# Kernel tuning notes

Hardware: AMD Instinct MI355X
Metric: run time of the kernel (lower is better)

Reference implementation:

```python
import jax, jax.numpy as jnp
import numpy as np

# Constants from init_kwargs
DT = 0.01
NIV = 8          # energy_input_dim[1]
HID = 64         # hidden_dims[0]
FEAT = 501       # per-field microstructure feature length (501+501=1002)


def _lin(k, fin, fout):
    return jax.random.normal(k, (fin, fout), dtype=jnp.float32) / np.sqrt(fin)


def setup_inputs() -> dict:
    key = jax.random.key(0)
    ks = jax.random.split(key, 12)
    B, T = 8192, 512
    e = jax.random.normal(ks[0], (B, T, 1), dtype=jnp.float32) * 0.1
    e_dot = jax.random.normal(ks[1], (B, T, 1), dtype=jnp.float32) * 0.1
    # positive microstructure fields (code computes nu**-1 and E/nu**2)
    E = jax.random.uniform(ks[2], (B, FEAT), minval=0.5, maxval=2.0, dtype=jnp.float32)
    nu = jax.random.uniform(ks[3], (B, FEAT), minval=0.5, maxval=2.0, dtype=jnp.float32)
    return {
        "e": e, "e_dot": e_dot, "E": E, "nu": nu,
        # EnergyFunction.B : Linear(1002,64) -> ReLU -> Linear(64,niv)
        "Bw1": _lin(ks[4], 2 * FEAT, HID), "Bb1": jnp.zeros((HID,), jnp.float32),
        "Bw2": _lin(ks[5], HID, NIV), "Bb2": jnp.zeros((NIV,), jnp.float32),
        # InverseDissipationPotential.beta : Linear(1002,64)->Softplus->Linear(64,niv)->Softplus
        "bw1": _lin(ks[6], 2 * FEAT, HID), "bb1": jnp.zeros((HID,), jnp.float32),
        "bw2": _lin(ks[7], HID, NIV), "bb2": jnp.zeros((NIV,), jnp.float32),
    }


def reference(e, e_dot, E, nu, Bw1, Bb1, Bw2, Bb2, bw1, bb1, bw2, bb2):
    # --- microstructure encoder (TrueFeatures) ---
    nu_p = 1.0 / jnp.mean(1.0 / nu, axis=1, keepdims=True)                 # [B,1]
    E_p = jnp.mean(E / nu ** 2, axis=1, keepdims=True) * nu_p ** 2         # [B,1]
    m = jnp.concatenate([E, nu], axis=-1)                                  # [B,1002]

    # Time-invariant MLP coefficients (hoisted out of the time loop)
    Bm = jax.nn.relu(m @ Bw1 + Bb1) @ Bw2 + Bb2                            # [B,NIV]
    beta = jax.nn.softplus(jax.nn.softplus(m @ bw1 + bb1) @ bw2 + bb2)     # [B,NIV]
    Bsum = jnp.sum(Bm, axis=-1, keepdims=True)                             # [B,1]

    B_, niv = Bm.shape
    xi0 = jnp.zeros((B_, niv), dtype=e.dtype)

    def step(xi, inp):
        u, p = inp                                                          # [B,1],[B,1]
        # Analytic gradients of L = sum_{b,k} Bm_bk * (0.5*E' u^2 + 0.5*(u-xi_k)^2 + 0.5*sum_j xi_j^2)
        du = u - xi                                                         # [B,NIV]
        grad_u = Bsum * E_p * u + jnp.sum(Bm * du, axis=-1, keepdims=True)  # [B,1] (s_eq)
        grad_v = -Bm * du + Bsum * xi                                       # [B,NIV] (d)
        q = -grad_v
        # Analytic gradients of potential = -0.5*nu' p^2 + 0.5*sum(beta*q^2)
        grad_p = -nu_p * p                                                  # [B,1] (s_neq)
        grad_q = beta * q                                                   # [B,NIV] (kinetics)
        stress = grad_u - grad_p
        return xi + DT * grad_q, (stress, xi)

    xs = (jnp.swapaxes(e, 0, 1), jnp.swapaxes(e_dot, 0, 1))                 # [T,B,1]
    _, (stress_t, xi_t) = jax.lax.scan(step, xi0, xs)
    stress = jnp.swapaxes(stress_t, 0, 1)                                   # [B,T,1]
    xi = jnp.swapaxes(xi_t, 0, 1)                                           # [B,T,NIV]
    return stress, xi
```

## Files before the change

kernel.cpp:

```cpp
#include <hip/hip_runtime.h>
#include <hip/hip_bf16.h>

#define FEATN 501
#define KPAD 1024
#define MSTRIDE 1032
#define NB 8192
#define NT 512
#define DTC 0.01f

typedef __attribute__((ext_vector_type(8))) short short8;
typedef __attribute__((ext_vector_type(4))) float f32x4;

__device__ __forceinline__ float softplus_f(float x) {
    return fmaxf(x, 0.f) + log1pf(expf(-fabsf(x)));
}
__device__ __forceinline__ ushort f2bf(float x) {
    __hip_bfloat16 h = __float2bfloat16(x);
    return *reinterpret_cast<ushort*>(&h);
}
__device__ __forceinline__ void gl_lds16(const void* g, void* l) {
    __builtin_amdgcn_global_load_lds(
        (const __attribute__((address_space(1))) void*)g,
        (__attribute__((address_space(3))) void*)l, 16, 0, 0);
}
__device__ __forceinline__ float dpp_add(float x, const int ctrl) {
    int s = __builtin_bit_cast(int, x);
    int y;
    switch (ctrl) {
    case 0xB1:  y = __builtin_amdgcn_update_dpp(0, s, 0xB1, 0xf, 0xf, true); break;
    case 0x4E:  y = __builtin_amdgcn_update_dpp(0, s, 0x4E, 0xf, 0xf, true); break;
    default:    y = __builtin_amdgcn_update_dpp(0, s, 0x141, 0xf, 0xf, true); break;
    }
    return x + __builtin_bit_cast(float, y);
}

__global__ __launch_bounds__(256) void wtrans_kernel(
    const float* __restrict__ Bw1, const float* __restrict__ bw1,
    ushort* __restrict__ Wt) {
    const int h = blockIdx.x;
    const float* W = (h < 64) ? Bw1 : bw1;
    const int col = h & 63;
    #pragma unroll
    for (int it = 0; it < 4; ++it) {
        const int k = it * 256 + threadIdx.x;
        const int ksrc = (k < FEATN) ? k
                       : (k >= 512 && k < 512 + FEATN) ? k - 11 : -1;
        const float v = (ksrc >= 0) ? W[(size_t)ksrc * 64 + col] : 0.f;
        Wt[(size_t)(((k >> 5) * 128 + h) * 4 + ((k >> 3) & 3)) * 8 + (k & 7)] =
            f2bf(v);
    }
}

__global__ __launch_bounds__(256, 8) void enc_kernel(
    const float* __restrict__ E, const float* __restrict__ nu,
    const ushort* __restrict__ Wt,
    const float* __restrict__ Bb1, const float* __restrict__ bb1,
    const float* __restrict__ Bw2, const float* __restrict__ Bb2,
    const float* __restrict__ bw2, const float* __restrict__ bb2,
    float* __restrict__ cw) {
    __shared__ ushort Ml[8 * MSTRIDE];
    __shared__ float hid[128][9];
    __shared__ float nups[8], Eps[8];

    const int tid = threadIdx.x;
    const int w = tid >> 6, lane = tid & 63;
    const int bb0 = blockIdx.x * 8;

    #pragma unroll
    for (int bp = 0; bp < 2; ++bp) {
        const int bl = w * 2 + bp;
        const size_t base = (size_t)(bb0 + bl) * FEATN;
        float s1 = 0.f, s2 = 0.f;
        for (int i = lane; i < FEATN; i += 64) {
            const float Ev = E[base + i];
            const float nv = nu[base + i];
            const float inv = 1.0f / nv;
            s1 += inv;
            s2 = fmaf(Ev, inv * inv, s2);
            Ml[bl * MSTRIDE + i] = f2bf(Ev);
            Ml[bl * MSTRIDE + 512 + i] = f2bf(nv);
        }
        if (lane < 11) {
            Ml[bl * MSTRIDE + FEATN + lane] = 0;
            Ml[bl * MSTRIDE + 512 + FEATN + lane] = 0;
        }
        #pragma unroll
        for (int o = 32; o; o >>= 1) {
            s1 += __shfl_xor(s1, o);
            s2 += __shfl_xor(s2, o);
        }
        if (lane == 0) {
            const float np = (float)FEATN / s1;
            nups[bl] = np;
            Eps[bl] = (s2 / (float)FEATN) * np * np;
        }
    }
    __syncthreads();

    const int r15 = lane & 15, kg = lane >> 4;
    {
        const ushort* wp = Wt + (size_t)(w * 32 + r15) * 32 + kg * 8;
        const int boff = (r15 & 7) * MSTRIDE + kg * 8;

        f32x4 acc0 = {0.f, 0.f, 0.f, 0.f}, acc1 = acc0;
        #pragma unroll 4
        for (int s = 0; s < 32; ++s) {
            const short8 a0 = *(const short8*)(wp + (size_t)s * 4096);
            const short8 a1 = *(const short8*)(wp + (size_t)s * 4096 + 512);
            const short8 b = *(const short8*)&Ml[boff + s * 32];
            acc0 = __builtin_amdgcn_mfma_f32_16x16x32_bf16(a0, b, acc0, 0, 0, 0);
            acc1 = __builtin_amdgcn_mfma_f32_16x16x32_bf16(a1, b, acc1, 0, 0, 0);
        }
        if (r15 < 8) {
            #pragma unroll
            for (int t = 0; t < 2; ++t) {
                #pragma unroll
                for (int r = 0; r < 4; ++r) {
                    const int h = w * 32 + t * 16 + kg * 4 + r;
                    const float bias = (h < 64) ? Bb1[h] : bb1[h - 64];
                    float v = (t ? acc1[r] : acc0[r]) + bias;
                    v = (h < 64) ? fmaxf(v, 0.f) : softplus_f(v);
                    hid[h][r15] = v;
                }
            }
        }
    }
    __syncthreads();

    if (tid < 64) {
        const int bl = tid >> 3, k = tid & 7;
        float dB = 0.f, db = 0.f;
        #pragma unroll 8
        for (int h = 0; h < 64; ++h) {
            dB = fmaf(hid[h][bl], Bw2[h * 8 + k], dB);
            db = fmaf(hid[64 + h][bl], bw2[h * 8 + k], db);
        }
        const float Bm = dB + Bb2[k];
        const float be = softplus_f(db + bb2[k]);
        float Bs = Bm;
        Bs += __shfl_xor(Bs, 1);
        Bs += __shfl_xor(Bs, 2);
        Bs += __shfl_xor(Bs, 4);
        float* cb = cw + (size_t)(bb0 + bl) * 32;
        cb[k] = 1.f - DTC * be * (Bm + Bs);
        cb[8 + k] = DTC * be * Bm;
        cb[16 + k] = Bm;
        if (k == 0) {
            cb[24] = Bs * (Eps[bl] + 1.f);
            cb[25] = nups[bl];
        }
    }
}

__global__ __launch_bounds__(256) void time_kernel(
    const float* __restrict__ e, const float* __restrict__ ed,
    const float* __restrict__ cw, float* __restrict__ stress,
    float* __restrict__ xi_out) {
    __shared__ float els[4][512];
    __shared__ float pls[4][512];
    const int wv = threadIdx.x >> 6;
    const int wid = (blockIdx.x << 2) + wv;
    const int lane = threadIdx.x & 63;
    const int j = lane >> 3, k = lane & 7;

    const float* eb = e + (size_t)wid * NT;
    const float* edb = ed + (size_t)wid * NT;
    gl_lds16(eb + lane * 4, &els[wv][0]);
    gl_lds16(eb + 256 + lane * 4, &els[wv][256]);
    gl_lds16(edb + lane * 4, &pls[wv][0]);
    gl_lds16(edb + 256 + lane * 4, &pls[wv][256]);

    const float* cb = cw + (size_t)wid * 32;
    const float a = cb[k];
    const float c = cb[8 + k];
    const float Bm = cb[16 + k];
    const float sE2 = cb[24];
    const float nup = cb[25];
    asm volatile("s_waitcnt vmcnt(0)" ::: "memory");

    const float a2 = a * a, a4 = a2 * a2;
    float A = 1.f;
    if (j & 1) A *= a;
    if (j & 2) A *= a2;
    if (j & 4) A *= a4;
    float pw[8];
    {
        float run = c;
        #pragma unroll
        for (int i = 7; i >= 0; --i) {
            const bool on = (i < j);
            pw[i] = on ? run : 0.f;
            run = on ? run * a : run;
        }
    }

    float* xb = xi_out + (size_t)wid * (NT * 8);
    float* sb = stress + (size_t)wid * NT;
    const float* el = &els[wv][0];
    const float* pl = &pls[wv][0];

    float xs = 0.f;
    #pragma unroll
    for (int it = 0; it < 64; ++it) {
        const int t0 = it * 8;
        const float4 q0 = *(const float4*)(el + t0);
        const float4 q1 = *(const float4*)(el + t0 + 4);
        const float cuj = el[t0 + j];
        const float cpj = pl[t0 + j];
        float xi_j = A * xs;
        xi_j = fmaf(pw[0], q0.x, xi_j);
        xi_j = fmaf(pw[1], q0.y, xi_j);
        xi_j = fmaf(pw[2], q0.z, xi_j);
        xi_j = fmaf(pw[3], q0.w, xi_j);
        xi_j = fmaf(pw[4], q1.x, xi_j);
        xi_j = fmaf(pw[5], q1.y, xi_j);
        xi_j = fmaf(pw[6], q1.z, xi_j);
        xi_j = fmaf(pw[7], q1.w, xi_j);
        xb[t0 * 8 + lane] = xi_j;
        float r = Bm * xi_j;
        r = dpp_add(r, 0xB1);
        r = dpp_add(r, 0x4E);
        r = dpp_add(r, 0x141);
        if (k == 0)
            sb[t0 + j] = fmaf(cuj, sE2, fmaf(nup, cpj, -r));
        xs = fmaf(a, __shfl(xi_j, 56 + k), c * q1.w);
    }
}

extern "C" void kernel_launch(void* const* d_in, const int* in_sizes, int n_in,
                              void* d_out, int out_size, void* d_ws, size_t ws_size,
                              hipStream_t stream) {
    const float* e   = (const float*)d_in[0];
    const float* ed  = (const float*)d_in[1];
    const float* E   = (const float*)d_in[2];
    const float* nu  = (const float*)d_in[3];
    const float* Bw1 = (const float*)d_in[4];
    const float* Bb1 = (const float*)d_in[5];
    const float* Bw2 = (const float*)d_in[6];
    const float* Bb2 = (const float*)d_in[7];
    const float* bw1 = (const float*)d_in[8];
    const float* bb1 = (const float*)d_in[9];
    const float* bw2 = (const float*)d_in[10];
    const float* bb2 = (const float*)d_in[11];

    float* out = (float*)d_out;
    float* stress = out;
    float* xi = out + (size_t)NB * NT;
    ushort* Wt = (ushort*)d_ws;
    float* cw = (float*)((char*)d_ws + (1 << 20));

    wtrans_kernel<<<128, 256, 0, stream>>>(Bw1, bw1, Wt);
    enc_kernel<<<1024, 256, 0, stream>>>(E, nu, Wt, Bb1, bb1,
                                         Bw2, Bb2, bw2, bb2, cw);
    time_kernel<<<2048, 256, 0, stream>>>(e, ed, cw, stress, xi);
}
```

Before: 69.29 us.

## Fuse encoder MLP and time-scan kernels into one per-block kernel

Merges the microstructure encoder and the time recurrence into a single kernel where each block handles four batch rows, passing coefficients through shared memory instead of a global workspace. Shared memory is aliased between the encoder staging buffers and the e/e_dot time-series buffers. The MFMA loop now wastes more of each 16-wide tile (only 4 of 16 columns used), and it rotates the K-slice start per block to spread weight reads. This removes a kernel launch and a global round trip, but doubles the per-row weight traffic and lowers the occupancy target.

```diff
diff --git a/kernel.cpp b/kernel.cpp
--- a/kernel.cpp
+++ b/kernel.cpp
@@ -2,8 +2,7 @@
 #include <hip/hip_bf16.h>
 
 #define FEATN 501
-#define KPAD 1024
-#define MSTRIDE 1032
+#define MST4 1032
 #define NB 8192
 #define NT 512
 #define DTC 0.01f
@@ -51,25 +50,29 @@
     }
 }
 
-__global__ __launch_bounds__(256, 8) void enc_kernel(
+__global__ __launch_bounds__(256, 6) void fused_kernel(
     const float* __restrict__ E, const float* __restrict__ nu,
     const ushort* __restrict__ Wt,
     const float* __restrict__ Bb1, const float* __restrict__ bb1,
     const float* __restrict__ Bw2, const float* __restrict__ Bb2,
     const float* __restrict__ bw2, const float* __restrict__ bb2,
-    float* __restrict__ cw) {
-    __shared__ ushort Ml[8 * MSTRIDE];
-    __shared__ float hid[128][9];
-    __shared__ float nups[8], Eps[8];
+    const float* __restrict__ e, const float* __restrict__ ed,
+    float* __restrict__ stress, float* __restrict__ xi_out) {
+    __shared__ __align__(16) char LDSU[16640];
+    ushort* Ml = (ushort*)LDSU;
+    float* hid = (float*)(LDSU + 8320);
+    float* els = (float*)LDSU;
+    float* pls = (float*)(LDSU + 8192);
+    __shared__ float coefL[4][32];
+    __shared__ float nups[4], Eps[4];
 
     const int tid = threadIdx.x;
     const int w = tid >> 6, lane = tid & 63;
-    const int bb0 = blockIdx.x * 8;
-
-    #pragma unroll
-    for (int bp = 0; bp < 2; ++bp) {
-        const int bl = w * 2 + bp;
-        const size_t base = (size_t)(bb0 + bl) * FEATN;
+    const int bb0 = blockIdx.x * 4;
+    const int r15 = lane & 15, kg = lane >> 4;
+
+    {
+        const size_t base = (size_t)(bb0 + w) * FEATN;
         float s1 = 0.f, s2 = 0.f;
         for (int i = lane; i < FEATN; i += 64) {
             const float Ev = E[base + i];
@@ -77,12 +80,12 @@
             const float inv = 1.0f / nv;
             s1 += inv;
             s2 = fmaf(Ev, inv * inv, s2);
-            Ml[bl * MSTRIDE + i] = f2bf(Ev);
-            Ml[bl * MSTRIDE + 512 + i] = f2bf(nv);
+            Ml[w * MST4 + i] = f2bf(Ev);
+            Ml[w * MST4 + 512 + i] = f2bf(nv);
         }
         if (lane < 11) {
-            Ml[bl * MSTRIDE + FEATN + lane] = 0;
-            Ml[bl * MSTRIDE + 512 + FEATN + lane] = 0;
+            Ml[w * MST4 + FEATN + lane] = 0;
+            Ml[w * MST4 + 512 + FEATN + lane] = 0;
         }
         #pragma unroll
         for (int o = 32; o; o >>= 1) {
@@ -91,27 +94,28 @@
         }
         if (lane == 0) {
             const float np = (float)FEATN / s1;
-            nups[bl] = np;
-            Eps[bl] = (s2 / (float)FEATN) * np * np;
+            nups[w] = np;
+            Eps[w] = (s2 / (float)FEATN) * np * np;
         }
     }
     __syncthreads();
 
-    const int r15 = lane & 15, kg = lane >> 4;
     {
-        const ushort* wp = Wt + (size_t)(w * 32 + r15) * 32 + kg * 8;
-        const int boff = (r15 & 7) * MSTRIDE + kg * 8;
+        const int aoff = (w * 32 + r15) * 32 + kg * 8;
+        const int boff = (r15 & 3) * MST4 + kg * 8;
+        const int rot = blockIdx.x & 31;
 
         f32x4 acc0 = {0.f, 0.f, 0.f, 0.f}, acc1 = acc0;
-        #pragma unroll 4
+        #pragma unroll 1
         for (int s = 0; s < 32; ++s) {
-            const short8 a0 = *(const short8*)(wp + (size_t)s * 4096);
-            const short8 a1 = *(const short8*)(wp + (size_t)s * 4096 + 512);
-            const short8 b = *(const short8*)&Ml[boff + s * 32];
+            const int ss = (s + rot) & 31;
+            const short8 a0 = *(const short8*)(Wt + ss * 4096 + aoff);
+            const short8 a1 = *(const short8*)(Wt + ss * 4096 + aoff + 512);
+            const short8 b = *(const short8*)&Ml[boff + ss * 32];
             acc0 = __builtin_amdgcn_mfma_f32_16x16x32_bf16(a0, b, acc0, 0, 0, 0);
             acc1 = __builtin_amdgcn_mfma_f32_16x16x32_bf16(a1, b, acc1, 0, 0, 0);
         }
-        if (r15 < 8) {
+        if (r15 < 4) {
             #pragma unroll
             for (int t = 0; t < 2; ++t) {
                 #pragma unroll
@@ -120,20 +124,20 @@
                     const float bias = (h < 64) ? Bb1[h] : bb1[h - 64];
                     float v = (t ? acc1[r] : acc0[r]) + bias;
                     v = (h < 64) ? fmaxf(v, 0.f) : softplus_f(v);
-                    hid[h][r15] = v;
+                    hid[h * 5 + r15] = v;
                 }
             }
         }
     }
     __syncthreads();
 
-    if (tid < 64) {
+    if (tid < 32) {
         const int bl = tid >> 3, k = tid & 7;
         float dB = 0.f, db = 0.f;
         #pragma unroll 8
         for (int h = 0; h < 64; ++h) {
-            dB = fmaf(hid[h][bl], Bw2[h * 8 + k], dB);
-            db = fmaf(hid[64 + h][bl], bw2[h * 8 + k], db);
+            dB = fmaf(hid[h * 5 + bl], Bw2[h * 8 + k], dB);
+            db = fmaf(hid[(64 + h) * 5 + bl], bw2[h * 8 + k], db);
         }
         const float Bm = dB + Bb2[k];
         const float be = softplus_f(db + bb2[k]);
@@ -141,89 +145,80 @@
         Bs += __shfl_xor(Bs, 1);
         Bs += __shfl_xor(Bs, 2);
         Bs += __shfl_xor(Bs, 4);
-        float* cb = cw + (size_t)(bb0 + bl) * 32;
-        cb[k] = 1.f - DTC * be * (Bm + Bs);
-        cb[8 + k] = DTC * be * Bm;
-        cb[16 + k] = Bm;
+        coefL[bl][k] = 1.f - DTC * be * (Bm + Bs);
+        coefL[bl][8 + k] = DTC * be * Bm;
+        coefL[bl][16 + k] = Bm;
         if (k == 0) {
-            cb[24] = Bs * (Eps[bl] + 1.f);
-            cb[25] = nups[bl];
-        }
-    }
-}
-
-__global__ __launch_bounds__(256) void time_kernel(
-    const float* __restrict__ e, const float* __restrict__ ed,
-    const float* __restrict__ cw, float* __restrict__ stress,
-    float* __restrict__ xi_out) {
-    __shared__ float els[4][512];
-    __shared__ float pls[4][512];
-    const int wv = threadIdx.x >> 6;
-    const int wid = (blockIdx.x << 2) + wv;
-    const int lane = threadIdx.x & 63;
-    const int j = lane >> 3, k = lane & 7;
-
-    const float* eb = e + (size_t)wid * NT;
-    const float* edb = ed + (size_t)wid * NT;
-    gl_lds16(eb + lane * 4, &els[wv][0]);
-    gl_lds16(eb + 256 + lane * 4, &els[wv][256]);
-    gl_lds16(edb + lane * 4, &pls[wv][0]);
-    gl_lds16(edb + 256 + lane * 4, &pls[wv][256]);
-
-    const float* cb = cw + (size_t)wid * 32;
-    const float a = cb[k];
-    const float c = cb[8 + k];
-    const float Bm = cb[16 + k];
-    const float sE2 = cb[24];
-    const float nup = cb[25];
-    asm volatile("s_waitcnt vmcnt(0)" ::: "memory");
-
-    const float a2 = a * a, a4 = a2 * a2;
-    float A = 1.f;
-    if (j & 1) A *= a;
-    if (j & 2) A *= a2;
-    if (j & 4) A *= a4;
-    float pw[8];
+            coefL[bl][24] = Bs * (Eps[bl] + 1.f);
+            coefL[bl][25] = nups[bl];
+        }
+    }
+    __syncthreads();
+
     {
-        float run = c;
+        const int wid = bb0 + w;
+        const int j = lane >> 3, k = lane & 7;
+        const float* eb = e + (size_t)wid * NT;
+        const float* edb = ed + (size_t)wid * NT;
+        float* el = els + w * 512;
+        float* pl = pls + w * 512;
+        gl_lds16(eb + lane * 4, el);
+        gl_lds16(eb + 256 + lane * 4, el + 256);
+        gl_lds16(edb + lane * 4, pl);
+        gl_lds16(edb + 256 + lane * 4, pl + 256);
+
+        const float a = coefL[w][k];
+        const float c = coefL[w][8 + k];
+        const float Bm = coefL[w][16 + k];
+        const float sE2 = coefL[w][24];
+        const float nup = coefL[w][25];
+        asm volatile("s_waitcnt vmcnt(0)" ::: "memory");
+
+        const float a2 = a * a, a4 = a2 * a2;
+        float A = 1.f;
+        if (j & 1) A *= a;
+        if (j & 2) A *= a2;
+        if (j & 4) A *= a4;
+        float pw[8];
+        {
+            float run = c;
+            #pragma unroll
+            for (int i = 7; i >= 0; --i) {
+                const bool on = (i < j);
+                pw[i] = on ? run : 0.f;
+                run = on ? run * a : run;
+            }
+        }
+
+        float* xb = xi_out + (size_t)wid * (NT * 8);
+        float* sb = stress + (size_t)wid * NT;
+
+        float xs = 0.f;
         #pragma unroll
-        for (int i = 7; i >= 0; --i) {
-            const bool on = (i < j);
-            pw[i] = on ? run : 0.f;
-            run = on ? run * a : run;
-        }
-    }
-
-    float* xb = xi_out + (size_t)wid * (NT * 8);
-    float* sb = stress + (size_t)wid * NT;
-    const float* el = &els[wv][0];
-    const float* pl = &pls[wv][0];
-
-    float xs = 0.f;
-    #pragma unroll
-    for (int it = 0; it < 64; ++it) {
-        const int t0 = it * 8;
-        const float4 q0 = *(const float4*)(el + t0);
-        const float4 q1 = *(const float4*)(el + t0 + 4);
-        const float cuj = el[t0 + j];
-        const float cpj = pl[t0 + j];
-        float xi_j = A * xs;
-        xi_j = fmaf(pw[0], q0.x, xi_j);
-        xi_j = fmaf(pw[1], q0.y, xi_j);
-        xi_j = fmaf(pw[2], q0.z, xi_j);
-        xi_j = fmaf(pw[3], q0.w, xi_j);
-        xi_j = fmaf(pw[4], q1.x, xi_j);
-        xi_j = fmaf(pw[5], q1.y, xi_j);
-        xi_j = fmaf(pw[6], q1.z, xi_j);
-        xi_j = fmaf(pw[7], q1.w, xi_j);
-        xb[t0 * 8 + lane] = xi_j;
-        float r = Bm * xi_j;
-        r = dpp_add(r, 0xB1);
-        r = dpp_add(r, 0x4E);
-        r = dpp_add(r, 0x141);
-        if (k == 0)
-            sb[t0 + j] = fmaf(cuj, sE2, fmaf(nup, cpj, -r));
-        xs = fmaf(a, __shfl(xi_j, 56 + k), c * q1.w);
+        for (int it = 0; it < 64; ++it) {
+            const int t0 = it * 8;
+            const float4 q0 = *(const float4*)(el + t0);
+            const float4 q1 = *(const float4*)(el + t0 + 4);
+            const float cuj = el[t0 + j];
+            const float cpj = pl[t0 + j];
+            float xi_j = A * xs;
+            xi_j = fmaf(pw[0], q0.x, xi_j);
+            xi_j = fmaf(pw[1], q0.y, xi_j);
+            xi_j = fmaf(pw[2], q0.z, xi_j);
+            xi_j = fmaf(pw[3], q0.w, xi_j);
+            xi_j = fmaf(pw[4], q1.x, xi_j);
+            xi_j = fmaf(pw[5], q1.y, xi_j);
+            xi_j = fmaf(pw[6], q1.z, xi_j);
+            xi_j = fmaf(pw[7], q1.w, xi_j);
+            xb[t0 * 8 + lane] = xi_j;
+            float r = Bm * xi_j;
+            r = dpp_add(r, 0xB1);
+            r = dpp_add(r, 0x4E);
+            r = dpp_add(r, 0x141);
+            if (k == 0)
+                sb[t0 + j] = fmaf(cuj, sE2, fmaf(nup, cpj, -r));
+            xs = fmaf(a, __shfl(xi_j, 56 + k), c * q1.w);
+        }
     }
 }
 
@@ -247,10 +242,9 @@
     float* stress = out;
     float* xi = out + (size_t)NB * NT;
     ushort* Wt = (ushort*)d_ws;
-    float* cw = (float*)((char*)d_ws + (1 << 20));
 
     wtrans_kernel<<<128, 256, 0, stream>>>(Bw1, bw1, Wt);
-    enc_kernel<<<1024, 256, 0, stream>>>(E, nu, Wt, Bb1, bb1,
-                                         Bw2, Bb2, bw2, bb2, cw);
-    time_kernel<<<2048, 256, 0, stream>>>(e, ed, cw, stress, xi);
-}
+    fused_kernel<<<2048, 256, 0, stream>>>(E, nu, Wt, Bb1, bb1,
+                                           Bw2, Bb2, bw2, bb2,
+                                           e, ed, stress, xi);
+}
```

Measured after the change: 78.42 us. 1.13x slower.
